# Performance work log

Measured on AMD Instinct MI355X. Metric: run time of the kernel, lower is better.

## Reference

```python
import jax, jax.numpy as jnp
import numpy as np

D_MODEL = 1024
N_HEADS = 16
HDIM = D_MODEL // N_HEADS
IMP_EPS = 1e-6


def setup_inputs() -> dict:
    key = jax.random.key(0)
    ks = jax.random.split(key, 7)
    B, T_q, T_kv, N_s = 2, 2048, 256, 16
    scale = 1.0 / np.sqrt(D_MODEL)
    return {
        "query": jax.random.normal(ks[0], (B, T_q, D_MODEL), dtype=jnp.float32),
        "key_value": jax.random.normal(ks[1], (B, T_kv, N_s, D_MODEL), dtype=jnp.float32),
        "imp_weights": jax.random.uniform(ks[2], (B, N_s), dtype=jnp.float32),
        "W_q": jax.random.normal(ks[3], (D_MODEL, D_MODEL), dtype=jnp.float32) * scale,
        "W_k": jax.random.normal(ks[4], (D_MODEL, D_MODEL), dtype=jnp.float32) * scale,
        "W_v": jax.random.normal(ks[5], (D_MODEL, D_MODEL), dtype=jnp.float32) * scale,
        "W_o": jax.random.normal(ks[6], (D_MODEL, D_MODEL), dtype=jnp.float32) * scale,
    }


def _split_heads(x):
    # [B, T, D] -> [B, h, T, d]
    B, T, _ = x.shape
    return x.reshape(B, T, N_HEADS, HDIM).transpose(0, 2, 1, 3)


def reference(query, key_value, imp_weights, W_q, W_k, W_v, W_o):
    # CAU_MultiheadCrossAttention.forward with 4D key_value (sensor axis).
    B, T_q, D = query.shape
    _, T_kv, N_s, _ = key_value.shape
    kv = key_value.reshape(B, T_kv * N_s, D)  # flatten sensor axis into source length S

    qh = _split_heads(query @ W_q.T)   # [B,h,T_q,d]  (nn.Linear: x @ W.T)
    kh = _split_heads(kv @ W_k.T)      # [B,h,S,d]
    vh = _split_heads(kv @ W_v.T)      # [B,h,S,d]

    # importance: [B,N_s] -> tiled over T_kv -> [B, S], log-clamped additive mask
    imp_full = jnp.broadcast_to(imp_weights[:, None, :], (B, T_kv, N_s)).reshape(B, T_kv * N_s)
    log_imp = jnp.log(jnp.clip(imp_full, IMP_EPS, None)).astype(qh.dtype)  # [B,S]

    scores = jnp.einsum("bhqd,bhkd->bhqk", qh, kh) / np.sqrt(HDIM).astype(np.float32)
    scores = scores + log_imp[:, None, None, :]
    attn = jax.nn.softmax(scores, axis=-1)
    y = jnp.einsum("bhqk,bhkd->bhqd", attn, vh)  # [B,h,T_q,d]

    y = y.transpose(0, 2, 1, 3).reshape(B, T_q, D)  # merge heads
    return y @ W_o.T
```

## Files before the change

### kernel.cpp

```cpp
#include <hip/hip_runtime.h>
#include <hip/hip_bf16.h>

typedef __bf16    bf16x8_t __attribute__((ext_vector_type(8)));
typedef __bf16    bf16x4_t __attribute__((ext_vector_type(4)));
typedef float     f32x4_t  __attribute__((ext_vector_type(4)));
typedef _Float16  f16x8_t  __attribute__((ext_vector_type(8)));

static __device__ __forceinline__ f32x4_t mfma16(bf16x8_t a, bf16x8_t b, f32x4_t c) {
    return __builtin_amdgcn_mfma_f32_16x16x32_bf16(a, b, c, 0, 0, 0);
}

static __device__ __forceinline__ float redsum16(float v) {
#pragma unroll
    for (int off = 1; off < 16; off <<= 1) v += __shfl_xor(v, off);
    return v;
}

static __device__ __forceinline__ void async16(const __bf16* g, __bf16* l) {
    __builtin_amdgcn_global_load_lds(
        (const __attribute__((address_space(1))) unsigned int*)g,
        (__attribute__((address_space(3))) unsigned int*)l, 16, 0, 0);
}

__global__ __launch_bounds__(256) void f2b_multi(const float* __restrict__ q,
                                                 const float* __restrict__ kv,
                                                 const float* __restrict__ wq,
                                                 const float* __restrict__ wk,
                                                 const float* __restrict__ wv,
                                                 const float* __restrict__ wo,
                                                 __bf16* __restrict__ qb,
                                                 __bf16* __restrict__ kvb,
                                                 __bf16* __restrict__ wqb,
                                                 __bf16* __restrict__ wkvb,
                                                 __bf16* __restrict__ wob,
                                                 float qscale) {
    int i = blockIdx.x * 256 + threadIdx.x;
    const float* src; __bf16* dst; int base; float scale = 1.0f;
    if (i < 1048576)      { src = q;  dst = qb;   base = 0; }
    else if (i < 3145728) { src = kv; dst = kvb;  base = 1048576; }
    else if (i < 3407872) { src = wq; dst = wqb;  base = 3145728; scale = qscale; }
    else if (i < 3670016) { src = wk; dst = wkvb; base = 3407872; }
    else if (i < 3932160) { src = wv; dst = wkvb + 1048576; base = 3670016; }
    else                  { src = wo; dst = wob;  base = 3932160; }
    int j = i - base;
    float4 v = reinterpret_cast<const float4*>(src)[j];
    bf16x4_t o;
    o[0] = (__bf16)(v.x * scale); o[1] = (__bf16)(v.y * scale);
    o[2] = (__bf16)(v.z * scale); o[3] = (__bf16)(v.w * scale);
    reinterpret_cast<bf16x4_t*>(dst)[j] = o;
}

__global__ __launch_bounds__(256) void proj_kernel(const __bf16* __restrict__ qb,
                                                   const __bf16* __restrict__ wqb,
                                                   const __bf16* __restrict__ kvb,
                                                   const __bf16* __restrict__ wkvb,
                                                   __bf16* __restrict__ Qp,
                                                   __bf16* __restrict__ Khd,
                                                   __bf16* __restrict__ Vhd,
                                                   const float* __restrict__ imp) {
    __shared__ __bf16 As[128 * 32];
    __shared__ __bf16 Bs[128 * 32];
    __shared__ __bf16 Es[2][4096];

    const int gid = blockIdx.x;
    const __bf16 *A, *B;
    long m0, n0;
    int mode;
    if (gid < 256) {
        m0 = (long)(gid >> 3) * 128; n0 = (long)(gid & 7) * 128;
        A = qb; B = wqb; mode = 0;
    } else {
        int g2 = gid - 256;
        m0 = (long)(g2 >> 4) * 128; n0 = (long)(g2 & 15) * 128;
        A = kvb; B = wkvb; mode = (n0 < 1024) ? 1 : 2;
    }

    const int t    = threadIdx.x;
    const int w    = t >> 6;
    const int lane = t & 63;
    const int quad = lane >> 4;
    const int mn   = lane & 15;
    const int wm   = (w & 1) * 64;
    const int wn   = (w >> 1) * 64;

    const int  srow = t >> 2;
    const int  scol = (t & 3) * 8;
    const __bf16* gA = A + (m0 + srow) * 1024 + scol;
    const __bf16* gB = B + (n0 + srow) * 1024 + scol;

    f32x4_t acc[4][4];
#pragma unroll
    for (int i = 0; i < 4; i++)
#pragma unroll
        for (int j = 0; j < 4; j++) acc[i][j] = (f32x4_t){0.f, 0.f, 0.f, 0.f};

    for (int k0 = 0; k0 < 1024; k0 += 32) {
        __syncthreads();
        async16(gA + k0,              &As[t * 8]);
        async16(gA + 64 * 1024 + k0,  &As[2048 + t * 8]);
        async16(gB + k0,              &Bs[t * 8]);
        async16(gB + 64 * 1024 + k0,  &Bs[2048 + t * 8]);
        __syncthreads();

        bf16x8_t af[4], bf[4];
#pragma unroll
        for (int i = 0; i < 4; i++)
            af[i] = *(const bf16x8_t*)&As[(wm + i * 16 + mn) * 32 + quad * 8];
#pragma unroll
        for (int j = 0; j < 4; j++)
            bf[j] = *(const bf16x8_t*)&Bs[(wn + j * 16 + mn) * 32 + quad * 8];
#pragma unroll
        for (int i = 0; i < 4; i++)
#pragma unroll
            for (int j = 0; j < 4; j++) acc[i][j] = mfma16(af[i], bf[j], acc[i][j]);
    }

    __syncthreads();
    __bf16* stg = (w == 0) ? As : (w == 1) ? Bs : Es[w - 2];

    if (mode != 2) {
#pragma unroll
        for (int i = 0; i < 4; i++)
#pragma unroll
            for (int j = 0; j < 4; j++)
#pragma unroll
                for (int r = 0; r < 4; r++) {
                    int sl = i * 16 + quad * 4 + r;
                    int d  = j * 16 + mn;
                    stg[sl * 64 + (((d >> 3) ^ (sl & 7)) * 8) + (d & 7)] =
                        (__bf16)acc[i][j][r];
                }
    } else {
        const int b_ = (int)((m0 + wm) >> 12);
#pragma unroll
        for (int r = 0; r < 4; r++) {
            float scl = fmaxf(imp[b_ * 16 + quad * 4 + r], 1e-6f);
#pragma unroll
            for (int j = 0; j < 4; j++) {
                bf16x4_t pk;
#pragma unroll
                for (int i = 0; i < 4; i++) pk[i] = (__bf16)(acc[i][j][r] * scl);
                int d  = j * 16 + mn;
                int p0 = (quad * 4 + r) * 4;
                *(bf16x4_t*)&stg[d * 64 + (((p0 >> 3) ^ (d & 7)) * 8) + (p0 & 7)] = pk;
            }
        }
    }

    if (mode == 0) {
        __bf16* Cg = Qp + (m0 + wm) * 1024 + (n0 + wn);
#pragma unroll
        for (int it = 0; it < 8; it++) {
            int rowL = it * 8 + (lane >> 3);
            int cb   = lane & 7;
            bf16x8_t vv = *(const bf16x8_t*)&stg[rowL * 64 + ((cb ^ (rowL & 7)) * 8)];
            *(bf16x8_t*)&Cg[(long)rowL * 1024 + cb * 8] = vv;
        }
    } else {
        const int b_    = (int)((m0 + wm) >> 12);
        const int sbase = (int)((m0 + wm) & 4095);
        __bf16* dst;
        if (mode == 1) {
            int h_ = (int)((n0 + wn) >> 6);
            dst = Khd + (long)(b_ * 16 + h_) * 262144 + (long)sbase * 64;
        } else {
            int h_ = (int)((n0 + wn) >> 6) - 16;
            dst = Vhd + (long)(b_ * 16 + h_) * 262144 + (long)(sbase >> 6) * 4096;
        }
#pragma unroll
        for (int it = 0; it < 8; it++) {
            int rowL = it * 8 + (lane >> 3);
            int cb   = lane & 7;
            bf16x8_t vv = *(const bf16x8_t*)&stg[rowL * 64 + ((cb ^ (rowL & 7)) * 8)];
            *(bf16x8_t*)&dst[rowL * 64 + cb * 8] = vv;
        }
    }
}

__global__ __launch_bounds__(256, 5) void attn_kernel(const __bf16* __restrict__ Qp,
                                                      const __bf16* __restrict__ Kh,
                                                      const __bf16* __restrict__ Vh,
                                                      const float* __restrict__ imp,
                                                      _Float16* __restrict__ Op,
                                                      float* __restrict__ Lp) {
    const int gid = blockIdx.x;
    const int qt  = (gid >> 3) & 31;
    const int sp  = (gid >> 8) & 1;
    const int bh  = ((gid >> 9) << 3) | (gid & 7);
    const int b   = bh >> 4;
    const int h   = bh & 15;
    const int t    = threadIdx.x;
    const int w    = t >> 6;
    const int lane = t & 63;
    const int quad = lane >> 4;
    const int mn   = lane & 15;

    __shared__ __bf16 Ks[2][64 * 64];
    __shared__ __bf16 Vs[64 * 64];
    __shared__ __bf16 Ps[4][16 * 64];

    const long qrow0 = (long)b * 2048 + qt * 64 + w * 16;
    const __bf16* Kb = Kh + (long)bh * 262144;
    const __bf16* Vb = Vh + (long)bh * 262144;

    const int r8 = lane >> 3;
    const int cs = (lane & 7) ^ r8;
    const int soff    = r8 * 64 + cs * 8;
    const int srcoff0 = (0 * 4 + w) * 512 + soff;
    const int srcoff1 = (1 * 4 + w) * 512 + soff;

    bf16x8_t aq[2];
#pragma unroll
    for (int x = 0; x < 2; x++)
        aq[x] = *(const bf16x8_t*)&Qp[(qrow0 + mn) * 1024 + h * 64 + x * 32 + quad * 8];

    const float impc = fmaxf(imp[b * 16 + mn], 1e-6f);

    float lpart[4];
    f32x4_t o[4];
#pragma unroll
    for (int r = 0; r < 4; r++) lpart[r] = 0.f;
#pragma unroll
    for (int dt = 0; dt < 4; dt++) o[dt] = (f32x4_t){0.f, 0.f, 0.f, 0.f};

    const int st0 = sp * 32;

    async16(Kb + (long)st0 * 4096 + srcoff0, &Ks[0][(0 * 4 + w) * 512]);
    async16(Kb + (long)st0 * 4096 + srcoff1, &Ks[0][(1 * 4 + w) * 512]);

    for (int it = 0; it < 32; ++it) {
        const int st  = st0 + it;
        const int cur = it & 1;

        __syncthreads();

        async16(Vb + (long)st * 4096 + srcoff0,       &Vs[(0 * 4 + w) * 512]);
        async16(Vb + (long)st * 4096 + srcoff1,       &Vs[(1 * 4 + w) * 512]);
        async16(Kb + (long)(st + 1) * 4096 + srcoff0, &Ks[cur ^ 1][(0 * 4 + w) * 512]);
        async16(Kb + (long)(st + 1) * 4096 + srcoff1, &Ks[cur ^ 1][(1 * 4 + w) * 512]);

        const __bf16* Kc = &Ks[cur][0];
        f32x4_t sc[4];
#pragma unroll
        for (int ct = 0; ct < 4; ct++) sc[ct] = (f32x4_t){0.f, 0.f, 0.f, 0.f};
        __builtin_amdgcn_s_setprio(1);
#pragma unroll
        for (int ct = 0; ct < 4; ct++) {
            int s  = ct * 16 + mn;
            int c0 = (quad ^ (s & 7)) * 8;
            bf16x8_t bk0 = *(const bf16x8_t*)&Kc[s * 64 + c0];
            bf16x8_t bk1 = *(const bf16x8_t*)&Kc[s * 64 + (c0 ^ 32)];
            sc[ct] = mfma16(aq[0], bk0, sc[ct]);
            sc[ct] = mfma16(aq[1], bk1, sc[ct]);
        }
        __builtin_amdgcn_s_setprio(0);

#pragma unroll
        for (int r = 0; r < 4; r++) {
            float p0 = __builtin_amdgcn_exp2f(sc[0][r]);
            float p1 = __builtin_amdgcn_exp2f(sc[1][r]);
            float p2 = __builtin_amdgcn_exp2f(sc[2][r]);
            float p3 = __builtin_amdgcn_exp2f(sc[3][r]);
            lpart[r] += (p0 + p1) + (p2 + p3);
            bf16x4_t pk;
            pk[0] = (__bf16)p0; pk[1] = (__bf16)p1;
            pk[2] = (__bf16)p2; pk[3] = (__bf16)p3;
            int row = quad * 4 + r;
            *(bf16x4_t*)&Ps[w][row * 64 + (((mn >> 1) ^ (row & 7)) * 8) + (mn & 1) * 4] = pk;
        }

        __syncthreads();

        {
            bf16x8_t bv0[4], bv1[4];
#pragma unroll
            for (int dt = 0; dt < 4; dt++) {
                int d  = dt * 16 + mn;
                int c0 = (quad ^ (d & 7)) * 8;
                bv0[dt] = *(const bf16x8_t*)&Vs[d * 64 + c0];
                bv1[dt] = *(const bf16x8_t*)&Vs[d * 64 + (c0 ^ 32)];
            }
            bf16x8_t ap0 = *(const bf16x8_t*)&Ps[w][mn * 64 + ((quad ^ (mn & 7)) * 8)];
            bf16x8_t ap1 = *(const bf16x8_t*)&Ps[w][mn * 64 + (((4 + quad) ^ (mn & 7)) * 8)];
            __builtin_amdgcn_s_setprio(1);
#pragma unroll
            for (int dt = 0; dt < 4; dt++) {
                o[dt] = mfma16(ap0, bv0[dt], o[dt]);
                o[dt] = mfma16(ap1, bv1[dt], o[dt]);
            }
            __builtin_amdgcn_s_setprio(0);
        }
    }

#pragma unroll
    for (int r = 0; r < 4; r++) {
        float l = redsum16(lpart[r] * impc);
        long row = qrow0 + quad * 4 + r;
        if (mn == 0) Lp[((long)sp * 4096 + row) * 16 + h] = l;
#pragma unroll
        for (int dt = 0; dt < 4; dt++)
            Op[((long)sp * 4096 + row) * 1024 + h * 64 + dt * 16 + mn] =
                (_Float16)o[dt][r];
    }
}

__global__ __launch_bounds__(256) void combine_kernel(const _Float16* __restrict__ Op,
                                                      const float* __restrict__ Lp,
                                                      __bf16* __restrict__ Y) {
    int tid = blockIdx.x * 256 + threadIdx.x;
    int row = tid >> 7;
    int cg  = tid & 127;
    int h   = cg >> 3;
    f16x8_t o0 = *(const f16x8_t*)&Op[(long)row * 1024 + cg * 8];
    f16x8_t o1 = *(const f16x8_t*)&Op[(long)(4096 + row) * 1024 + cg * 8];
    float inv = 1.0f / (Lp[row * 16 + h] + Lp[(4096 + row) * 16 + h]);
    bf16x8_t y;
#pragma unroll
    for (int j = 0; j < 8; j++) y[j] = (__bf16)(((float)o0[j] + (float)o1[j]) * inv);
    *(bf16x8_t*)&Y[(long)row * 1024 + cg * 8] = y;
}

__global__ __launch_bounds__(256) void gemm_out_kernel(const __bf16* __restrict__ A,
                                                       const __bf16* __restrict__ B,
                                                       float* __restrict__ P) {
    __shared__ __bf16 As[128 * 32];
    __shared__ __bf16 Bs[128 * 32];

    const int  kh = blockIdx.x >> 3;
    const long n0 = (long)(blockIdx.x & 7) * 128;
    const long m0 = (long)blockIdx.y * 128;
    const int  kb = kh * 512;
    float* C = P + (long)kh * 4194304;

    const int t    = threadIdx.x;
    const int w    = t >> 6;
    const int lane = t & 63;
    const int quad = lane >> 4;
    const int mn   = lane & 15;
    const int wm   = (w & 1) * 64;
    const int wn   = (w >> 1) * 64;

    const int  srow = t >> 2;
    const int  scol = (t & 3) * 8;
    const __bf16* gA = A + (m0 + srow) * 1024 + kb + scol;
    const __bf16* gB = B + (n0 + srow) * 1024 + kb + scol;

    f32x4_t acc[4][4];
#pragma unroll
    for (int i = 0; i < 4; i++)
#pragma unroll
        for (int j = 0; j < 4; j++) acc[i][j] = (f32x4_t){0.f, 0.f, 0.f, 0.f};

    for (int k0 = 0; k0 < 512; k0 += 32) {
        __syncthreads();
        async16(gA + k0,             &As[t * 8]);
        async16(gA + 64 * 1024 + k0, &As[2048 + t * 8]);
        async16(gB + k0,             &Bs[t * 8]);
        async16(gB + 64 * 1024 + k0, &Bs[2048 + t * 8]);
        __syncthreads();

        bf16x8_t af[4], bf[4];
#pragma unroll
        for (int i = 0; i < 4; i++)
            af[i] = *(const bf16x8_t*)&As[(wm + i * 16 + mn) * 32 + quad * 8];
#pragma unroll
        for (int j = 0; j < 4; j++)
            bf[j] = *(const bf16x8_t*)&Bs[(wn + j * 16 + mn) * 32 + quad * 8];
#pragma unroll
        for (int i = 0; i < 4; i++)
#pragma unroll
            for (int j = 0; j < 4; j++) acc[i][j] = mfma16(af[i], bf[j], acc[i][j]);
    }

#pragma unroll
    for (int i = 0; i < 4; i++)
#pragma unroll
        for (int j = 0; j < 4; j++)
#pragma unroll
            for (int r = 0; r < 4; r++) {
                long row = m0 + wm + i * 16 + quad * 4 + r;
                long col = n0 + wn + j * 16 + mn;
                C[row * 1024 + col] = acc[i][j][r];
            }
}

__global__ __launch_bounds__(256) void combine2_kernel(const float* __restrict__ P0,
                                                       const float* __restrict__ P1,
                                                       float* __restrict__ out) {
    int i = blockIdx.x * 256 + threadIdx.x;
    float4 a = reinterpret_cast<const float4*>(P0)[i];
    float4 b = reinterpret_cast<const float4*>(P1)[i];
    float4 c; c.x = a.x + b.x; c.y = a.y + b.y; c.z = a.z + b.z; c.w = a.w + b.w;
    reinterpret_cast<float4*>(out)[i] = c;
}

extern "C" void kernel_launch(void* const* d_in, const int* in_sizes, int n_in,
                              void* d_out, int out_size, void* d_ws, size_t ws_size,
                              hipStream_t stream) {
    const float* q_f  = (const float*)d_in[0];
    const float* kv_f = (const float*)d_in[1];
    const float* imp  = (const float*)d_in[2];
    const float* wq_f = (const float*)d_in[3];
    const float* wk_f = (const float*)d_in[4];
    const float* wv_f = (const float*)d_in[5];
    const float* wo_f = (const float*)d_in[6];

    char* ws = (char*)d_ws;
    const size_t MB = 1ull << 20;
    __bf16*   qb    = (__bf16*)(ws + 0);
    __bf16*   kvb   = (__bf16*)(ws + 8 * MB);
    __bf16*   wqb   = (__bf16*)(ws + 24 * MB);
    __bf16*   wkvb  = (__bf16*)(ws + 26 * MB);
    _Float16* Opart = (_Float16*)(ws + 0);
    float*    Lpart = (float*)(ws + 16 * MB);
    __bf16*   Yb    = (__bf16*)(ws + 17 * MB);
    __bf16*   wob   = (__bf16*)(ws + 30 * MB);
    __bf16*   Qp    = (__bf16*)(ws + 32 * MB);
    __bf16*   Khd   = (__bf16*)(ws + 40 * MB);
    __bf16*   Vhd   = (__bf16*)(ws + 56 * MB);
    float*    Gp    = (float*)(ws + 40 * MB);

    const float QSCALE = 0.125f * 1.4426950408889634f;

    f2b_multi<<<16384, 256, 0, stream>>>(q_f, kv_f, wq_f, wk_f, wv_f, wo_f,
                                         qb, kvb, wqb, wkvb, wob, QSCALE);

    proj_kernel<<<1280, 256, 0, stream>>>(qb, wqb, kvb, wkvb, Qp, Khd, Vhd, imp);

    attn_kernel<<<2048, 256, 0, stream>>>(Qp, Khd, Vhd, imp, Opart, Lpart);
    combine_kernel<<<2048, 256, 0, stream>>>(Opart, Lpart, Yb);

    gemm_out_kernel<<<dim3(16, 32), 256, 0, stream>>>(Yb, wob, Gp);
    combine2_kernel<<<4096, 256, 0, stream>>>(Gp, Gp + 4194304, (float*)d_out);
}
```

Measured before the change: 309.9 us.

## Rewrite attention with 32x32 MFMA, register-resident P via permlane32 swap

The attention kernel moves from 16x16x32 to 32x32x16 bf16 MFMA tiles, so each wave handles 32 query rows and each block 128 rows, which halves the grid. It computes S^T (K as the A operand) so the exponentiated probabilities can be rearranged into the PV operand layout with permlane32_swap, removing the per-wave LDS staging buffer for P. The K prefetch moves after the mid-iteration barrier, and the V projection epilogue store is reordered to write along the sequence axis. The cost is more registers per wave (occupancy hint drops from 5 to 4) and fewer blocks for the GPU to schedule.

```diff
diff --git a/kernel.cpp b/kernel.cpp
--- a/kernel.cpp
+++ b/kernel.cpp
@@ -4,16 +4,22 @@
 typedef __bf16    bf16x8_t __attribute__((ext_vector_type(8)));
 typedef __bf16    bf16x4_t __attribute__((ext_vector_type(4)));
 typedef float     f32x4_t  __attribute__((ext_vector_type(4)));
+typedef float     f32x16_t __attribute__((ext_vector_type(16)));
 typedef _Float16  f16x8_t  __attribute__((ext_vector_type(8)));
+typedef unsigned int u32x2_t __attribute__((ext_vector_type(2)));
+typedef unsigned int u32x4_t __attribute__((ext_vector_type(4)));
 
 static __device__ __forceinline__ f32x4_t mfma16(bf16x8_t a, bf16x8_t b, f32x4_t c) {
     return __builtin_amdgcn_mfma_f32_16x16x32_bf16(a, b, c, 0, 0, 0);
 }
-
-static __device__ __forceinline__ float redsum16(float v) {
-#pragma unroll
-    for (int off = 1; off < 16; off <<= 1) v += __shfl_xor(v, off);
-    return v;
+static __device__ __forceinline__ f32x16_t mfma32(bf16x8_t a, bf16x8_t b, f32x16_t c) {
+    return __builtin_amdgcn_mfma_f32_32x32x16_bf16(a, b, c, 0, 0, 0);
+}
+static __device__ __forceinline__ f32x16_t zero16() {
+    f32x16_t z;
+#pragma unroll
+    for (int j = 0; j < 16; j++) z[j] = 0.f;
+    return z;
 }
 
 static __device__ __forceinline__ void async16(const __bf16* g, __bf16* l) {
@@ -132,19 +138,21 @@
                 }
     } else {
         const int b_ = (int)((m0 + wm) >> 12);
-#pragma unroll
-        for (int r = 0; r < 4; r++) {
-            float scl = fmaxf(imp[b_ * 16 + quad * 4 + r], 1e-6f);
+        float scl[4];
+#pragma unroll
+        for (int r = 0; r < 4; r++)
+            scl[r] = fmaxf(imp[b_ * 16 + quad * 4 + r], 1e-6f);
+#pragma unroll
+        for (int i = 0; i < 4; i++)
 #pragma unroll
             for (int j = 0; j < 4; j++) {
                 bf16x4_t pk;
 #pragma unroll
-                for (int i = 0; i < 4; i++) pk[i] = (__bf16)(acc[i][j][r] * scl);
+                for (int r = 0; r < 4; r++) pk[r] = (__bf16)(acc[i][j][r] * scl[r]);
                 int d  = j * 16 + mn;
-                int p0 = (quad * 4 + r) * 4;
-                *(bf16x4_t*)&stg[d * 64 + (((p0 >> 3) ^ (d & 7)) * 8) + (p0 & 7)] = pk;
+                int s0 = i * 16 + quad * 4;
+                *(bf16x4_t*)&stg[d * 64 + (((s0 >> 3) ^ (d & 7)) * 8) + (s0 & 7)] = pk;
             }
-        }
     }
 
     if (mode == 0) {
@@ -177,29 +185,28 @@
     }
 }
 
-__global__ __launch_bounds__(256, 5) void attn_kernel(const __bf16* __restrict__ Qp,
+__global__ __launch_bounds__(256, 4) void attn_kernel(const __bf16* __restrict__ Qp,
                                                       const __bf16* __restrict__ Kh,
                                                       const __bf16* __restrict__ Vh,
                                                       const float* __restrict__ imp,
                                                       _Float16* __restrict__ Op,
                                                       float* __restrict__ Lp) {
     const int gid = blockIdx.x;
-    const int qt  = (gid >> 3) & 31;
-    const int sp  = (gid >> 8) & 1;
-    const int bh  = ((gid >> 9) << 3) | (gid & 7);
+    const int qt  = (gid >> 3) & 15;
+    const int sp  = (gid >> 7) & 1;
+    const int bh  = ((gid >> 8) << 3) | (gid & 7);
     const int b   = bh >> 4;
     const int h   = bh & 15;
     const int t    = threadIdx.x;
     const int w    = t >> 6;
     const int lane = t & 63;
-    const int quad = lane >> 4;
-    const int mn   = lane & 15;
+    const int hi   = lane >> 5;
+    const int q32  = lane & 31;
 
     __shared__ __bf16 Ks[2][64 * 64];
     __shared__ __bf16 Vs[64 * 64];
-    __shared__ __bf16 Ps[4][16 * 64];
-
-    const long qrow0 = (long)b * 2048 + qt * 64 + w * 16;
+
+    const long qrow0 = (long)b * 2048 + qt * 128 + w * 32;
     const __bf16* Kb = Kh + (long)bh * 262144;
     const __bf16* Vb = Vh + (long)bh * 262144;
 
@@ -209,24 +216,24 @@
     const int srcoff0 = (0 * 4 + w) * 512 + soff;
     const int srcoff1 = (1 * 4 + w) * 512 + soff;
 
-    bf16x8_t aq[2];
-#pragma unroll
-    for (int x = 0; x < 2; x++)
-        aq[x] = *(const bf16x8_t*)&Qp[(qrow0 + mn) * 1024 + h * 64 + x * 32 + quad * 8];
-
-    const float impc = fmaxf(imp[b * 16 + mn], 1e-6f);
-
-    float lpart[4];
-    f32x4_t o[4];
-#pragma unroll
-    for (int r = 0; r < 4; r++) lpart[r] = 0.f;
-#pragma unroll
-    for (int dt = 0; dt < 4; dt++) o[dt] = (f32x4_t){0.f, 0.f, 0.f, 0.f};
+    bf16x8_t aq[4];
+#pragma unroll
+    for (int ks = 0; ks < 4; ks++)
+        aq[ks] = *(const bf16x8_t*)&Qp[(qrow0 + q32) * 1024 + h * 64 + ks * 16 + hi * 8];
+
+    float lp[2][4];
+#pragma unroll
+    for (int j = 0; j < 2; j++)
+#pragma unroll
+        for (int r = 0; r < 4; r++) lp[j][r] = 0.f;
+    f32x16_t o0 = zero16(), o1 = zero16();
 
     const int st0 = sp * 32;
 
     async16(Kb + (long)st0 * 4096 + srcoff0, &Ks[0][(0 * 4 + w) * 512]);
     async16(Kb + (long)st0 * 4096 + srcoff1, &Ks[0][(1 * 4 + w) * 512]);
+
+    const int sw8 = q32 & 7;
 
     for (int it = 0; it < 32; ++it) {
         const int st  = st0 + it;
@@ -234,73 +241,84 @@
 
         __syncthreads();
 
-        async16(Vb + (long)st * 4096 + srcoff0,       &Vs[(0 * 4 + w) * 512]);
-        async16(Vb + (long)st * 4096 + srcoff1,       &Vs[(1 * 4 + w) * 512]);
+        async16(Vb + (long)st * 4096 + srcoff0, &Vs[(0 * 4 + w) * 512]);
+        async16(Vb + (long)st * 4096 + srcoff1, &Vs[(1 * 4 + w) * 512]);
+
+        const __bf16* Kc = &Ks[cur][0];
+        bf16x8_t pa[4];
+
+#pragma unroll
+        for (int st2 = 0; st2 < 2; st2++) {
+            f32x16_t sc = zero16();
+            __builtin_amdgcn_s_setprio(1);
+#pragma unroll
+            for (int ks = 0; ks < 4; ks++) {
+                bf16x8_t kf = *(const bf16x8_t*)
+                    &Kc[(st2 * 32 + q32) * 64 + ((((ks << 1) | hi) ^ sw8) << 3)];
+                sc = mfma32(kf, aq[ks], sc);
+            }
+            __builtin_amdgcn_s_setprio(0);
+
+            unsigned int wv[8];
+#pragma unroll
+            for (int g = 0; g < 4; g++) {
+                float p0 = __builtin_amdgcn_exp2f(sc[4 * g + 0]);
+                float p1 = __builtin_amdgcn_exp2f(sc[4 * g + 1]);
+                float p2 = __builtin_amdgcn_exp2f(sc[4 * g + 2]);
+                float p3 = __builtin_amdgcn_exp2f(sc[4 * g + 3]);
+                lp[g & 1][0] += p0; lp[g & 1][1] += p1;
+                lp[g & 1][2] += p2; lp[g & 1][3] += p3;
+                bf16x4_t pk;
+                pk[0] = (__bf16)p0; pk[1] = (__bf16)p1;
+                pk[2] = (__bf16)p2; pk[3] = (__bf16)p3;
+                u32x2_t uu = __builtin_bit_cast(u32x2_t, pk);
+                wv[2 * g]     = uu[0];
+                wv[2 * g + 1] = uu[1];
+            }
+            u32x2_t s02 = __builtin_amdgcn_permlane32_swap(wv[0], wv[2], false, false);
+            u32x2_t s13 = __builtin_amdgcn_permlane32_swap(wv[1], wv[3], false, false);
+            u32x2_t s46 = __builtin_amdgcn_permlane32_swap(wv[4], wv[6], false, false);
+            u32x2_t s57 = __builtin_amdgcn_permlane32_swap(wv[5], wv[7], false, false);
+            u32x4_t pu0 = {s02[0], s13[0], s02[1], s13[1]};
+            u32x4_t pu1 = {s46[0], s57[0], s46[1], s57[1]};
+            pa[st2 * 2 + 0] = __builtin_bit_cast(bf16x8_t, pu0);
+            pa[st2 * 2 + 1] = __builtin_bit_cast(bf16x8_t, pu1);
+        }
+
+        __syncthreads();
+
         async16(Kb + (long)(st + 1) * 4096 + srcoff0, &Ks[cur ^ 1][(0 * 4 + w) * 512]);
         async16(Kb + (long)(st + 1) * 4096 + srcoff1, &Ks[cur ^ 1][(1 * 4 + w) * 512]);
 
-        const __bf16* Kc = &Ks[cur][0];
-        f32x4_t sc[4];
-#pragma unroll
-        for (int ct = 0; ct < 4; ct++) sc[ct] = (f32x4_t){0.f, 0.f, 0.f, 0.f};
         __builtin_amdgcn_s_setprio(1);
 #pragma unroll
-        for (int ct = 0; ct < 4; ct++) {
-            int s  = ct * 16 + mn;
-            int c0 = (quad ^ (s & 7)) * 8;
-            bf16x8_t bk0 = *(const bf16x8_t*)&Kc[s * 64 + c0];
-            bf16x8_t bk1 = *(const bf16x8_t*)&Kc[s * 64 + (c0 ^ 32)];
-            sc[ct] = mfma16(aq[0], bk0, sc[ct]);
-            sc[ct] = mfma16(aq[1], bk1, sc[ct]);
+        for (int ks = 0; ks < 4; ks++) {
+            bf16x8_t v0 = *(const bf16x8_t*)
+                &Vs[(0 * 32 + q32) * 64 + ((((ks << 1) | hi) ^ sw8) << 3)];
+            bf16x8_t v1 = *(const bf16x8_t*)
+                &Vs[(1 * 32 + q32) * 64 + ((((ks << 1) | hi) ^ sw8) << 3)];
+            o0 = mfma32(pa[ks], v0, o0);
+            o1 = mfma32(pa[ks], v1, o1);
         }
         __builtin_amdgcn_s_setprio(0);
-
-#pragma unroll
-        for (int r = 0; r < 4; r++) {
-            float p0 = __builtin_amdgcn_exp2f(sc[0][r]);
-            float p1 = __builtin_amdgcn_exp2f(sc[1][r]);
-            float p2 = __builtin_amdgcn_exp2f(sc[2][r]);
-            float p3 = __builtin_amdgcn_exp2f(sc[3][r]);
-            lpart[r] += (p0 + p1) + (p2 + p3);
-            bf16x4_t pk;
-            pk[0] = (__bf16)p0; pk[1] = (__bf16)p1;
-            pk[2] = (__bf16)p2; pk[3] = (__bf16)p3;
-            int row = quad * 4 + r;
-            *(bf16x4_t*)&Ps[w][row * 64 + (((mn >> 1) ^ (row & 7)) * 8) + (mn & 1) * 4] = pk;
-        }
-
-        __syncthreads();
-
-        {
-            bf16x8_t bv0[4], bv1[4];
-#pragma unroll
-            for (int dt = 0; dt < 4; dt++) {
-                int d  = dt * 16 + mn;
-                int c0 = (quad ^ (d & 7)) * 8;
-                bv0[dt] = *(const bf16x8_t*)&Vs[d * 64 + c0];
-                bv1[dt] = *(const bf16x8_t*)&Vs[d * 64 + (c0 ^ 32)];
-            }
-            bf16x8_t ap0 = *(const bf16x8_t*)&Ps[w][mn * 64 + ((quad ^ (mn & 7)) * 8)];
-            bf16x8_t ap1 = *(const bf16x8_t*)&Ps[w][mn * 64 + (((4 + quad) ^ (mn & 7)) * 8)];
-            __builtin_amdgcn_s_setprio(1);
-#pragma unroll
-            for (int dt = 0; dt < 4; dt++) {
-                o[dt] = mfma16(ap0, bv0[dt], o[dt]);
-                o[dt] = mfma16(ap1, bv1[dt], o[dt]);
-            }
-            __builtin_amdgcn_s_setprio(0);
-        }
-    }
-
-#pragma unroll
-    for (int r = 0; r < 4; r++) {
-        float l = redsum16(lpart[r] * impc);
-        long row = qrow0 + quad * 4 + r;
-        if (mn == 0) Lp[((long)sp * 4096 + row) * 16 + h] = l;
-#pragma unroll
-        for (int dt = 0; dt < 4; dt++)
-            Op[((long)sp * 4096 + row) * 1024 + h * 64 + dt * 16 + mn] =
-                (_Float16)o[dt][r];
+    }
+
+    float lsum = 0.f;
+#pragma unroll
+    for (int j = 0; j < 2; j++)
+#pragma unroll
+        for (int r = 0; r < 4; r++)
+            lsum += lp[j][r] * fmaxf(imp[b * 16 + 4 * hi + 8 * j + r], 1e-6f);
+    lsum += __shfl_xor(lsum, 32);
+    if (lane < 32)
+        Lp[((long)sp * 4096 + qrow0 + q32) * 16 + h] = lsum;
+
+#pragma unroll
+    for (int j = 0; j < 16; j++) {
+        int q_loc = (j & 3) + 8 * (j >> 2) + 4 * hi;
+        long row  = (long)sp * 4096 + qrow0 + q_loc;
+        Op[row * 1024 + h * 64 + 0 * 32 + q32] = (_Float16)o0[j];
+        Op[row * 1024 + h * 64 + 1 * 32 + q32] = (_Float16)o1[j];
     }
 }
 
@@ -427,7 +445,7 @@
 
     proj_kernel<<<1280, 256, 0, stream>>>(qb, wqb, kvb, wkvb, Qp, Khd, Vhd, imp);
 
-    attn_kernel<<<2048, 256, 0, stream>>>(Qp, Khd, Vhd, imp, Opart, Lpart);
+    attn_kernel<<<1024, 256, 0, stream>>>(Qp, Khd, Vhd, imp, Opart, Lpart);
     combine_kernel<<<2048, 256, 0, stream>>>(Opart, Lpart, Yb);
 
     gemm_out_kernel<<<dim3(16, 32), 256, 0, stream>>>(Yb, wob, Gp);
```

New measurement: 292.1 us. 1.06x faster.
